# Kernel optimization log

Hardware: AMD Instinct MI355X
Metric: run time of the kernel (lower is better)

Reference implementation:

```python
import jax, jax.numpy as jnp
import numpy as np

NEG_SLOPE = 0.2
EPS = 1e-16


def gat_layer(x, edge_index, edge_attr, W, We, a_src, a_dst, a_edge, bias,
              add_self_loops):
    """PyG GATConv with concat=True.
    x: [N, F_in], edge_index: [2, E] (row 0 = src j, row 1 = dst i),
    edge_attr: [E, De], W: [F_in, H*C], We: [De, H*C],
    a_src/a_dst/a_edge: [H, C], bias: [H*C].
    """
    N = x.shape[0]
    H, C = a_src.shape
    if add_self_loops:
        # fill_value='mean': self-loop edge_attr = mean of incoming edge_attr per node
        dst0 = edge_index[1]
        s = jax.ops.segment_sum(edge_attr, dst0, num_segments=N)
        cnt = jax.ops.segment_sum(jnp.ones((edge_attr.shape[0], 1), edge_attr.dtype),
                                  dst0, num_segments=N)
        loop_attr = s / jnp.maximum(cnt, 1.0)
        loop_idx = jnp.arange(N, dtype=edge_index.dtype)
        edge_index = jnp.concatenate(
            [edge_index, jnp.stack([loop_idx, loop_idx])], axis=1)
        edge_attr = jnp.concatenate([edge_attr, loop_attr], axis=0)

    src, dst = edge_index[0], edge_index[1]
    h = (x @ W).reshape(N, H, C)                       # [N, H, C]
    e = (edge_attr @ We).reshape(-1, H, C)             # [E, H, C]

    alpha_src = jnp.einsum('nhc,hc->nh', h, a_src)     # [N, H]
    alpha_dst = jnp.einsum('nhc,hc->nh', h, a_dst)     # [N, H]
    alpha_edge = jnp.einsum('ehc,hc->eh', e, a_edge)   # [E, H]

    alpha = alpha_src[src] + alpha_dst[dst] + alpha_edge
    alpha = jax.nn.leaky_relu(alpha, NEG_SLOPE)

    # segment softmax over destination node
    amax = jax.ops.segment_max(alpha, dst, num_segments=N)      # [N, H]
    ex = jnp.exp(alpha - amax[dst])
    denom = jax.ops.segment_sum(ex, dst, num_segments=N)        # [N, H]
    attn = ex / (denom[dst] + EPS)                               # [E, H]

    msg = h[src] * attn[:, :, None]                              # [E, H, C]
    out = jax.ops.segment_sum(msg, dst, num_segments=N)          # [N, H, C]
    return out.reshape(N, H * C) + bias


def setup_inputs() -> dict:
    key = jax.random.key(0)
    ks = jax.random.split(key, 16)
    N, E, F_in, C, H, De = 10000, 160000, 128, 64, 8, 1
    d1 = H * C  # 512

    def glorot(k, shape):
        fan = shape[0] + shape[-1]
        s = jnp.sqrt(6.0 / fan)
        return jax.random.uniform(k, shape, jnp.float32, -s, s)

    return {
        'x': jax.random.normal(ks[0], (N, F_in), jnp.float32),
        'edge_index': jax.random.randint(ks[1], (2, E), 0, N, jnp.int32),
        'edge_attr': jax.random.normal(ks[2], (E, De), jnp.float32),
        # layer 1 params
        'W1': glorot(ks[3], (F_in, d1)),
        'We1': glorot(ks[4], (De, d1)),
        'as1': glorot(ks[5], (H, C)),
        'ad1': glorot(ks[6], (H, C)),
        'ae1': glorot(ks[7], (H, C)),
        'b1': jnp.zeros((d1,), jnp.float32),
        # layer 2 params
        'W2': glorot(ks[8], (d1, d1)),
        'We2': glorot(ks[9], (De, d1)),
        'as2': glorot(ks[10], (H, C)),
        'ad2': glorot(ks[11], (H, C)),
        'ae2': glorot(ks[12], (H, C)),
        'b2': jnp.zeros((d1,), jnp.float32),
    }


def reference(x, edge_index, edge_attr,
              W1, We1, as1, ad1, ae1, b1,
              W2, We2, as2, ad2, ae2, b2):
    h = gat_layer(x, edge_index, edge_attr, W1, We1, as1, ad1, ae1, b1,
                  add_self_loops=False)
    h = jax.nn.relu(h)
    h = gat_layer(h, edge_index, edge_attr, W2, We2, as2, ad2, ae2, b2,
                  add_self_loops=True)
    return jnp.mean(h, axis=0)  # [512]
```

## Files before the change

### kernel.cpp

```cpp
#include <hip/hip_runtime.h>
#include <hip/hip_bf16.h>

#define HD __device__ __forceinline__
typedef unsigned short u16;
typedef __attribute__((ext_vector_type(8))) short bf16x8;
typedef __attribute__((ext_vector_type(4))) float f32x4;

HD u16 f2b(float f){
  unsigned u = __float_as_uint(f);
  unsigned r = (u + 0x7fffu + ((u>>16)&1u)) >> 16;
  return (u16)r;
}
HD float b2f(short s){ return __uint_as_float(((unsigned)(u16)s)<<16); }

__global__ void k_count(const int* __restrict__ dst, const float* __restrict__ ea,
                        int* cnt, float* easum, int E){
  int e = blockIdx.x*blockDim.x + threadIdx.x;
  if (e>=E) return;
  int d = dst[e];
  atomicAdd(&cnt[d],1);
  atomicAdd(&easum[d], ea[e]);
}

__global__ __launch_bounds__(1024) void k_scan(const int* __restrict__ cnt, int* offs, int N){
  __shared__ int lds[1024];
  const int chunk = (N + 1023)/1024;
  const int b = threadIdx.x*chunk;
  int s = 0;
  for (int i=0;i<chunk;++i){ int idx=b+i; if (idx<N) s += cnt[idx]; }
  lds[threadIdx.x] = s;
  __syncthreads();
  #pragma unroll
  for (int off=1; off<1024; off<<=1){
    int t = (threadIdx.x>=(unsigned)off)? lds[threadIdx.x-off] : 0;
    __syncthreads();
    lds[threadIdx.x] += t;
    __syncthreads();
  }
  int excl = lds[threadIdx.x] - s;
  for (int i=0;i<chunk;++i){
    int idx=b+i;
    if (idx<N){ offs[idx] = excl; excl += cnt[idx]; }
  }
  if (threadIdx.x==1023) offs[N] = lds[1023];
}

__global__ void k_scatter(const int* __restrict__ src, const int* __restrict__ dst,
                          const float* __restrict__ ea, const int* __restrict__ offs,
                          int* fill, int* srcs, float* eas, int E){
  int e = blockIdx.x*blockDim.x + threadIdx.x;
  if (e>=E) return;
  int d = dst[e];
  int p = offs[d] + atomicAdd(&fill[d],1);
  srcs[p] = src[e];
  eas[p]  = ea[e];
}

__global__ __launch_bounds__(512) void k_prep_small(
    const int* __restrict__ cnt, const float* __restrict__ easum, float* la, int N,
    const float* __restrict__ We1, const float* __restrict__ ae1,
    const float* __restrict__ We2, const float* __restrict__ ae2,
    float* wedot, int nbLoop){
  int bx = blockIdx.x;
  if (bx < nbLoop){
    int n = bx*512 + threadIdx.x;
    if (n<N) la[n] = easum[n] / fmaxf((float)cnt[n], 1.f);
    return;
  }
  int which = bx - nbLoop;
  const float* We = which? We2 : We1;
  const float* ae = which? ae2 : ae1;
  int hh = threadIdx.x>>6, lane = threadIdx.x&63;
  float p = We[hh*64+lane]*ae[hh*64+lane];
  #pragma unroll
  for (int o=32;o;o>>=1) p += __shfl_down(p,o);
  if (lane==0) wedot[which*8+hh] = p;
}

__global__ __launch_bounds__(256) void k_prep_cast(
    const float* __restrict__ x, u16* __restrict__ xb, int total4,
    const float* __restrict__ W1, u16* __restrict__ W1t,
    const float* __restrict__ W2, u16* __restrict__ W2t,
    int nbCast, int nbW1){
  __shared__ float T[64][65];
  int bx = blockIdx.x;
  if (bx < nbCast){
    int i = bx*256 + threadIdx.x;
    if (i<total4){
      float4 v = *(const float4*)(x + (size_t)i*4);
      ushort4 o; o.x=f2b(v.x); o.y=f2b(v.y); o.z=f2b(v.z); o.w=f2b(v.w);
      *(ushort4*)(xb + (size_t)i*4) = o;
    }
    return;
  }
  const float* W; u16* Wt; int K, Nn, t;
  if (bx < nbCast + nbW1){ t = bx - nbCast;        W = W1; Wt = W1t; K = 128; Nn = 512; }
  else                   { t = bx - nbCast - nbW1; W = W2; Wt = W2t; K = 512; Nn = 512; }
  int nt = Nn/64;
  int k0 = (t/nt)*64, n0 = (t%nt)*64;
  #pragma unroll
  for (int i=0;i<16;++i){
    int id = i*256 + threadIdx.x;
    int r = id>>6, c = id&63;
    T[r][c] = W[(size_t)(k0+r)*Nn + n0 + c];
  }
  __syncthreads();
  #pragma unroll
  for (int i=0;i<16;++i){
    int id = i*256 + threadIdx.x;
    int rr = id>>6, cc = id&63;
    Wt[(size_t)(n0+rr)*K + k0 + cc] = f2b(T[cc][rr]);
  }
}

__global__ __launch_bounds__(256) void k_gemm_mfma(
    const u16* __restrict__ A, const u16* __restrict__ Bt,
    u16* __restrict__ Cb,
    const float* __restrict__ a_s, const float* __restrict__ a_d,
    float* __restrict__ asrc, float* __restrict__ adst,
    int M, int N, int K){
  __shared__ char lds[256*80];
  char* As = lds;
  char* Bs = lds + 128*80;
  const int tid = threadIdx.x;
  const int lane = tid & 63, w = tid >> 6;
  const int wr = w >> 1, wc = w & 1;
  const int l15 = lane & 15, l4 = lane >> 4;
  const int m0 = blockIdx.y*128, n0 = blockIdx.x*128;

  f32x4 acc[4][4] = {};
  int aoff[4], boff[4];
  #pragma unroll
  for (int i=0;i<4;++i) aoff[i] = (wr*64 + i*16 + l15)*80 + l4*16;
  #pragma unroll
  for (int j=0;j<4;++j) boff[j] = (wc*64 + j*16 + l15)*80 + l4*16;

  for (int k0=0; k0<K; k0+=32){
    #pragma unroll
    for (int i=0;i<2;++i){
      int cid = tid*2+i;
      int r = cid>>2, c = cid&3;
      int row = m0 + r;
      float4 v = make_float4(0.f,0.f,0.f,0.f);
      if (row < M) v = *(const float4*)(A + (size_t)row*K + k0 + c*8);
      *(float4*)(As + r*80 + c*16) = v;
    }
    #pragma unroll
    for (int i=0;i<2;++i){
      int cid = tid*2+i;
      int r = cid>>2, c = cid&3;
      float4 v = *(const float4*)(Bt + (size_t)(n0+r)*K + k0 + c*8);
      *(float4*)(Bs + r*80 + c*16) = v;
    }
    __syncthreads();
    bf16x8 a[4], b[4];
    #pragma unroll
    for (int i=0;i<4;++i) a[i] = *reinterpret_cast<const bf16x8*>(As + aoff[i]);
    #pragma unroll
    for (int j=0;j<4;++j) b[j] = *reinterpret_cast<const bf16x8*>(Bs + boff[j]);
    #pragma unroll
    for (int i=0;i<4;++i)
      #pragma unroll
      for (int j=0;j<4;++j)
        acc[i][j] = __builtin_amdgcn_mfma_f32_16x16x32_bf16(a[i], b[j], acc[i][j], 0,0,0);
    __syncthreads();
  }

  const int head = (n0>>6) + wc;
  float sv[4][4] = {}, dv[4][4] = {};
  #pragma unroll
  for (int i=0;i<4;++i){
    #pragma unroll
    for (int j=0;j<4;++j){
      int col = n0 + wc*64 + j*16 + l15;
      float asv = a_s[col], adv = a_d[col];
      #pragma unroll
      for (int r=0;r<4;++r){
        int row = m0 + wr*64 + i*16 + l4*4 + r;
        u16 bits = f2b(acc[i][j][r]);
        float valf = b2f((short)bits);
        if (row < M) Cb[(size_t)row*N + col] = bits;
        sv[i][r] = fmaf(valf, asv, sv[i][r]);
        dv[i][r] = fmaf(valf, adv, dv[i][r]);
      }
    }
  }
  #pragma unroll
  for (int i=0;i<4;++i){
    #pragma unroll
    for (int r=0;r<4;++r){
      float s_ = sv[i][r], d_ = dv[i][r];
      #pragma unroll
      for (int mask=1; mask<16; mask<<=1){
        s_ += __shfl_xor(s_, mask);
        d_ += __shfl_xor(d_, mask);
      }
      if (l15==0){
        int row = m0 + wr*64 + i*16 + l4*4 + r;
        if (row < M){ asrc[row*8+head] = s_; adst[row*8+head] = d_; }
      }
    }
  }
}

__global__ __launch_bounds__(256) void k_flashagg(const u16* __restrict__ hb,
    const int* __restrict__ srcs, const float* __restrict__ eas,
    const int* __restrict__ offs,
    const float* __restrict__ asrc, const float* __restrict__ adst,
    const float* __restrict__ wedot, const float* __restrict__ la,
    const float* __restrict__ bias,
    u16* __restrict__ outb,
    int N, int relu_flag, int self_flag){
  int n = blockIdx.x*4 + (threadIdx.x>>6);
  if (n>=N) return;
  int lane = threadIdx.x&63;
  int hh = lane&7, esub = lane>>3;
  int ahh = lane>>3;
  int c0 = lane*8;
  int beg = offs[n], end = offs[n+1];
  float wd = wedot[hh];
  float adn = adst[n*8+hh];

  float aselfa = -1e30f;
  if (self_flag){
    float a = asrc[n*8+hh] + adn + la[n]*wd;
    aselfa = a>0.f ? a : 0.2f*a;
  }
  float aself_c = __shfl(aselfa, ahh);

  float m = self_flag ? aself_c : -1e30f;
  float s = 0.f;
  float acc[8] = {};

  for (int p0=beg; p0<end; p0+=16){
    int pA = p0 + esub, pB = p0 + 8 + esub;
    float aA = -1e30f, aB = -1e30f;
    int sA = 0, sB = 0;
    if (pA < end){
      sA = srcs[pA];
      float eaA = eas[pA];
      float a = asrc[sA*8+hh] + adn + eaA*wd;
      aA = a>0.f ? a : 0.2f*a;
    }
    if (pB < end){
      sB = srcs[pB];
      float eaB = eas[pB];
      float a = asrc[sB*8+hh] + adn + eaB*wd;
      aB = a>0.f ? a : 0.2f*a;
    }
    float av[16]; int se[16];
    #pragma unroll
    for (int e=0;e<8;++e){ av[e]   = __shfl(aA, e*8 + ahh); se[e]   = __shfl(sA, e*8); }
    #pragma unroll
    for (int e=0;e<8;++e){ av[8+e] = __shfl(aB, e*8 + ahh); se[8+e] = __shfl(sB, e*8); }
    float mo = m;
    #pragma unroll
    for (int e=0;e<16;++e) mo = fmaxf(mo, av[e]);
    float f = __expf(m - mo);
    m = mo;
    s *= f;
    #pragma unroll
    for (int j=0;j<8;++j) acc[j] *= f;
    #pragma unroll
    for (int e=0;e<16;++e){
      if (p0 + e < end){
        float ee = __expf(av[e] - m);
        s += ee;
        bf16x8 v = *(const bf16x8*)(hb + (size_t)se[e]*512 + c0);
        #pragma unroll
        for (int j=0;j<8;++j) acc[j] = fmaf(ee, b2f(v[j]), acc[j]);
      }
    }
  }
  if (self_flag){
    float xs = __expf(aself_c - m);
    s += xs;
    bf16x8 v = *(const bf16x8*)(hb + (size_t)n*512 + c0);
    #pragma unroll
    for (int j=0;j<8;++j) acc[j] = fmaf(xs, b2f(v[j]), acc[j]);
  }
  float iv = 1.f/(s + 1e-16f);
  bf16x8 ov;
  #pragma unroll
  for (int j=0;j<8;++j){
    float val = acc[j]*iv + bias[c0+j];
    if (relu_flag) val = fmaxf(val, 0.f);
    ov[j] = (short)f2b(val);
  }
  *(bf16x8*)(outb + (size_t)n*512 + c0) = ov;
}

__global__ __launch_bounds__(512) void k_colmean(const u16* __restrict__ out2b,
                          float* __restrict__ o, int N, float invN){
  int c = threadIdx.x;
  int n0 = blockIdx.x*16;
  int nend = min(n0+16, N);
  float s = 0.f;
  for (int n=n0;n<nend;++n) s += b2f(out2b[(size_t)n*512 + c]);
  atomicAdd(&o[c], s*invN);
}

extern "C" void kernel_launch(void* const* d_in, const int* in_sizes, int n_in,
                              void* d_out, int out_size, void* d_ws, size_t ws_size,
                              hipStream_t stream){
  const float* x   = (const float*)d_in[0];
  const int* eidx  = (const int*)d_in[1];
  const float* ea  = (const float*)d_in[2];
  const float* W1  = (const float*)d_in[3];
  const float* We1 = (const float*)d_in[4];
  const float* as1 = (const float*)d_in[5];
  const float* ad1 = (const float*)d_in[6];
  const float* ae1 = (const float*)d_in[7];
  const float* b1  = (const float*)d_in[8];
  const float* W2  = (const float*)d_in[9];
  const float* We2 = (const float*)d_in[10];
  const float* as2 = (const float*)d_in[11];
  const float* ad2 = (const float*)d_in[12];
  const float* ae2 = (const float*)d_in[13];
  const float* b2  = (const float*)d_in[14];
  float* outp = (float*)d_out;

  const int FIN = 128, D1 = 512;
  const int N = in_sizes[0]/FIN;
  const int E = in_sizes[1]/2;
  const int* srcA = eidx;
  const int* dstA = eidx + E;

  char* ws = (char*)d_ws;
  size_t o = 0;
  auto alloc = [&](size_t bytes)->void*{
    void* p = ws + o; o = (o + bytes + 255) & ~(size_t)255; return p;
  };
  u16*   hb1   = (u16*)  alloc((size_t)N*D1*2);
  u16*   hb2   = (u16*)  alloc((size_t)N*D1*2);
  u16*   out1rb= (u16*)  alloc((size_t)N*D1*2);
  u16*   out2b = (u16*)  alloc((size_t)N*D1*2);
  u16*   xb    = (u16*)  alloc((size_t)N*FIN*2);
  u16*   W1t   = (u16*)  alloc((size_t)D1*FIN*2);
  u16*   W2t   = (u16*)  alloc((size_t)D1*D1*2);
  int*   srcs  = (int*)  alloc((size_t)E*4);
  float* eas   = (float*)alloc((size_t)E*4);
  int*   offs  = (int*)  alloc((size_t)(N+1)*4);
  size_t zbeg = o;
  int*   cnt   = (int*)  alloc((size_t)N*4);
  int*   fill  = (int*)  alloc((size_t)N*4);
  float* easum = (float*)alloc((size_t)N*4);
  size_t zend = o;
  float* asrc  = (float*)alloc((size_t)N*8*4);
  float* adst  = (float*)alloc((size_t)N*8*4);
  float* la    = (float*)alloc((size_t)N*4);
  float* wedot = (float*)alloc(64);
  (void)ws_size; (void)n_in;

  hipMemsetAsync(ws + zbeg, 0, zend - zbeg, stream);
  hipMemsetAsync(d_out, 0, (size_t)out_size*sizeof(float), stream);

  dim3 b256(256);
  int ge = (E+255)/256;
  int gn4 = (N+3)/4;

  k_count   <<<ge, b256, 0, stream>>>(dstA, ea, cnt, easum, E);
  k_scan    <<<1, 1024, 0, stream>>>(cnt, offs, N);
  k_scatter <<<ge, b256, 0, stream>>>(srcA, dstA, ea, offs, fill, srcs, eas, E);
  {
    int nbLoop = (N+511)/512;
    k_prep_small<<<nbLoop+2, 512, 0, stream>>>(cnt, easum, la, N,
                                               We1, ae1, We2, ae2, wedot, nbLoop);
    int total4 = N*FIN/4;
    int nbCast = (total4+255)/256;
    int nbW1 = (FIN/64)*(D1/64);
    int nbW2 = (D1/64)*(D1/64);
    k_prep_cast<<<nbCast+nbW1+nbW2, b256, 0, stream>>>(x, xb, total4,
                                                       W1, W1t, W2, W2t, nbCast, nbW1);
  }

  k_gemm_mfma<<<dim3(D1/128, (N+127)/128), b256, 0, stream>>>(
      xb, W1t, hb1, as1, ad1, asrc, adst, N, D1, FIN);
  k_flashagg<<<gn4, b256, 0, stream>>>(hb1, srcs, eas, offs, asrc, adst, wedot, la,
                                       b1, out1rb, N, 1, 0);

  k_gemm_mfma<<<dim3(D1/128, (N+127)/128), b256, 0, stream>>>(
      out1rb, W2t, hb2, as2, ad2, asrc, adst, N, D1, D1);
  k_flashagg<<<gn4, b256, 0, stream>>>(hb2, srcs, eas, offs, asrc, adst, wedot+8, la,
                                       b2, out2b, N, 0, 1);

  k_colmean<<<(N+15)/16, 512, 0, stream>>>(out2b, outp, N, 1.0f/(float)N);
}
```

Measured before the change: 179.8 us.

## Merge prep kernels and fuse x bf16 cast into first GEMM load

Merges edge counting, weight transpose/cast and wedot computation into one launch, and runs the scan, loop-attr mean and first GEMM together in a second launch. The first GEMM now reads fp32 x directly and rounds to bf16 while staging tiles, which removes the separate cast pass and the xb buffer. The scan shrinks to a single 256-thread block inside the heterogeneous launch, so it does less parallel work per element and can become the longest block. The aim is to cut launch count and serial dependencies in the preprocessing phase.

```diff
diff --git a/kernel.cpp b/kernel.cpp
--- a/kernel.cpp
+++ b/kernel.cpp
@@ -13,120 +13,19 @@
 }
 HD float b2f(short s){ return __uint_as_float(((unsigned)(u16)s)<<16); }
 
-__global__ void k_count(const int* __restrict__ dst, const float* __restrict__ ea,
-                        int* cnt, float* easum, int E){
-  int e = blockIdx.x*blockDim.x + threadIdx.x;
-  if (e>=E) return;
-  int d = dst[e];
-  atomicAdd(&cnt[d],1);
-  atomicAdd(&easum[d], ea[e]);
-}
-
-__global__ __launch_bounds__(1024) void k_scan(const int* __restrict__ cnt, int* offs, int N){
-  __shared__ int lds[1024];
-  const int chunk = (N + 1023)/1024;
-  const int b = threadIdx.x*chunk;
-  int s = 0;
-  for (int i=0;i<chunk;++i){ int idx=b+i; if (idx<N) s += cnt[idx]; }
-  lds[threadIdx.x] = s;
-  __syncthreads();
-  #pragma unroll
-  for (int off=1; off<1024; off<<=1){
-    int t = (threadIdx.x>=(unsigned)off)? lds[threadIdx.x-off] : 0;
-    __syncthreads();
-    lds[threadIdx.x] += t;
-    __syncthreads();
-  }
-  int excl = lds[threadIdx.x] - s;
-  for (int i=0;i<chunk;++i){
-    int idx=b+i;
-    if (idx<N){ offs[idx] = excl; excl += cnt[idx]; }
-  }
-  if (threadIdx.x==1023) offs[N] = lds[1023];
-}
-
-__global__ void k_scatter(const int* __restrict__ src, const int* __restrict__ dst,
-                          const float* __restrict__ ea, const int* __restrict__ offs,
-                          int* fill, int* srcs, float* eas, int E){
-  int e = blockIdx.x*blockDim.x + threadIdx.x;
-  if (e>=E) return;
-  int d = dst[e];
-  int p = offs[d] + atomicAdd(&fill[d],1);
-  srcs[p] = src[e];
-  eas[p]  = ea[e];
-}
-
-__global__ __launch_bounds__(512) void k_prep_small(
-    const int* __restrict__ cnt, const float* __restrict__ easum, float* la, int N,
-    const float* __restrict__ We1, const float* __restrict__ ae1,
-    const float* __restrict__ We2, const float* __restrict__ ae2,
-    float* wedot, int nbLoop){
-  int bx = blockIdx.x;
-  if (bx < nbLoop){
-    int n = bx*512 + threadIdx.x;
-    if (n<N) la[n] = easum[n] / fmaxf((float)cnt[n], 1.f);
-    return;
-  }
-  int which = bx - nbLoop;
-  const float* We = which? We2 : We1;
-  const float* ae = which? ae2 : ae1;
-  int hh = threadIdx.x>>6, lane = threadIdx.x&63;
-  float p = We[hh*64+lane]*ae[hh*64+lane];
-  #pragma unroll
-  for (int o=32;o;o>>=1) p += __shfl_down(p,o);
-  if (lane==0) wedot[which*8+hh] = p;
-}
-
-__global__ __launch_bounds__(256) void k_prep_cast(
-    const float* __restrict__ x, u16* __restrict__ xb, int total4,
-    const float* __restrict__ W1, u16* __restrict__ W1t,
-    const float* __restrict__ W2, u16* __restrict__ W2t,
-    int nbCast, int nbW1){
-  __shared__ float T[64][65];
-  int bx = blockIdx.x;
-  if (bx < nbCast){
-    int i = bx*256 + threadIdx.x;
-    if (i<total4){
-      float4 v = *(const float4*)(x + (size_t)i*4);
-      ushort4 o; o.x=f2b(v.x); o.y=f2b(v.y); o.z=f2b(v.z); o.w=f2b(v.w);
-      *(ushort4*)(xb + (size_t)i*4) = o;
-    }
-    return;
-  }
-  const float* W; u16* Wt; int K, Nn, t;
-  if (bx < nbCast + nbW1){ t = bx - nbCast;        W = W1; Wt = W1t; K = 128; Nn = 512; }
-  else                   { t = bx - nbCast - nbW1; W = W2; Wt = W2t; K = 512; Nn = 512; }
-  int nt = Nn/64;
-  int k0 = (t/nt)*64, n0 = (t%nt)*64;
-  #pragma unroll
-  for (int i=0;i<16;++i){
-    int id = i*256 + threadIdx.x;
-    int r = id>>6, c = id&63;
-    T[r][c] = W[(size_t)(k0+r)*Nn + n0 + c];
-  }
-  __syncthreads();
-  #pragma unroll
-  for (int i=0;i<16;++i){
-    int id = i*256 + threadIdx.x;
-    int rr = id>>6, cc = id&63;
-    Wt[(size_t)(n0+rr)*K + k0 + cc] = f2b(T[cc][rr]);
-  }
-}
-
-__global__ __launch_bounds__(256) void k_gemm_mfma(
-    const u16* __restrict__ A, const u16* __restrict__ Bt,
-    u16* __restrict__ Cb,
-    const float* __restrict__ a_s, const float* __restrict__ a_d,
-    float* __restrict__ asrc, float* __restrict__ adst,
-    int M, int N, int K){
-  __shared__ char lds[256*80];
+template<int AF32>
+HD void gemm_body(const void* Ap, const u16* __restrict__ Bt,
+                  u16* __restrict__ Cb,
+                  const float* __restrict__ a_s, const float* __restrict__ a_d,
+                  float* __restrict__ asrc, float* __restrict__ adst,
+                  int M, int N, int K, int bidx, int bidy, char* lds){
   char* As = lds;
   char* Bs = lds + 128*80;
   const int tid = threadIdx.x;
   const int lane = tid & 63, w = tid >> 6;
   const int wr = w >> 1, wc = w & 1;
   const int l15 = lane & 15, l4 = lane >> 4;
-  const int m0 = blockIdx.y*128, n0 = blockIdx.x*128;
+  const int m0 = bidy*128, n0 = bidx*128;
 
   f32x4 acc[4][4] = {};
   int aoff[4], boff[4];
@@ -141,9 +40,24 @@
       int cid = tid*2+i;
       int r = cid>>2, c = cid&3;
       int row = m0 + r;
-      float4 v = make_float4(0.f,0.f,0.f,0.f);
-      if (row < M) v = *(const float4*)(A + (size_t)row*K + k0 + c*8);
-      *(float4*)(As + r*80 + c*16) = v;
+      if (AF32){
+        const float* A = (const float*)Ap;
+        float4 v0 = make_float4(0.f,0.f,0.f,0.f), v1 = v0;
+        if (row < M){
+          v0 = *(const float4*)(A + (size_t)row*K + k0 + c*8);
+          v1 = *(const float4*)(A + (size_t)row*K + k0 + c*8 + 4);
+        }
+        ushort4 o0, o1;
+        o0.x=f2b(v0.x); o0.y=f2b(v0.y); o0.z=f2b(v0.z); o0.w=f2b(v0.w);
+        o1.x=f2b(v1.x); o1.y=f2b(v1.y); o1.z=f2b(v1.z); o1.w=f2b(v1.w);
+        *(ushort4*)(As + r*80 + c*16)     = o0;
+        *(ushort4*)(As + r*80 + c*16 + 8) = o1;
+      } else {
+        const u16* A = (const u16*)Ap;
+        float4 v = make_float4(0.f,0.f,0.f,0.f);
+        if (row < M) v = *(const float4*)(A + (size_t)row*K + k0 + c*8);
+        *(float4*)(As + r*80 + c*16) = v;
+      }
     }
     #pragma unroll
     for (int i=0;i<2;++i){
@@ -201,6 +115,125 @@
       }
     }
   }
+}
+
+__global__ __launch_bounds__(256) void k_prepA(
+    const int* __restrict__ dst, const float* __restrict__ ea,
+    int* cnt, float* easum, int E, int nbCount,
+    const float* __restrict__ W1, u16* __restrict__ W1t,
+    const float* __restrict__ W2, u16* __restrict__ W2t,
+    const float* __restrict__ We1, const float* __restrict__ ae1,
+    const float* __restrict__ We2, const float* __restrict__ ae2,
+    float* wedot){
+  __shared__ float T[64][65];
+  int bx = blockIdx.x;
+  int tid = threadIdx.x;
+  if (bx < nbCount){
+    int e = bx*256 + tid;
+    if (e<E){
+      int d = dst[e];
+      atomicAdd(&cnt[d],1);
+      atomicAdd(&easum[d], ea[e]);
+    }
+    return;
+  }
+  bx -= nbCount;
+  if (bx < 16 + 64){
+    const float* W; u16* Wt; int K, t;
+    if (bx < 16){ t = bx;      W = W1; Wt = W1t; K = 128; }
+    else        { t = bx - 16; W = W2; Wt = W2t; K = 512; }
+    const int Nn = 512, nt = 8;
+    int k0 = (t/nt)*64, n0 = (t%nt)*64;
+    #pragma unroll
+    for (int i=0;i<16;++i){
+      int id = i*256 + tid;
+      int r = id>>6, c = id&63;
+      T[r][c] = W[(size_t)(k0+r)*Nn + n0 + c];
+    }
+    __syncthreads();
+    #pragma unroll
+    for (int i=0;i<16;++i){
+      int id = i*256 + tid;
+      int rr = id>>6, cc = id&63;
+      Wt[(size_t)(n0+rr)*K + k0 + cc] = f2b(T[cc][rr]);
+    }
+    return;
+  }
+  int idx = bx - 80;
+  int which = idx>>1, hg = idx&1;
+  const float* We = which? We2 : We1;
+  const float* ae = which? ae2 : ae1;
+  int wv = tid>>6, lane = tid&63;
+  int head = hg*4 + wv;
+  float p = We[head*64+lane]*ae[head*64+lane];
+  #pragma unroll
+  for (int o=32;o;o>>=1) p += __shfl_down(p,o);
+  if (lane==0) wedot[which*8+head] = p;
+}
+
+__global__ __launch_bounds__(256) void k_prepB(
+    const int* __restrict__ cnt, int* offs, int N, int nbLa,
+    const float* __restrict__ easum, float* la,
+    const float* __restrict__ x, const u16* __restrict__ W1t,
+    u16* __restrict__ hb1,
+    const float* __restrict__ a_s, const float* __restrict__ a_d,
+    float* __restrict__ asrc, float* __restrict__ adst,
+    int M, int Nd, int K){
+  __shared__ char glds[256*80];
+  __shared__ int slds[256];
+  int bx = blockIdx.x;
+  int tid = threadIdx.x;
+  if (bx == 0){
+    const int chunk = (N + 255)/256;
+    const int b = tid*chunk;
+    int s = 0;
+    for (int i=0;i<chunk;++i){ int idx=b+i; if (idx<N) s += cnt[idx]; }
+    slds[tid] = s;
+    __syncthreads();
+    #pragma unroll
+    for (int off=1; off<256; off<<=1){
+      int t = (tid>=off)? slds[tid-off] : 0;
+      __syncthreads();
+      slds[tid] += t;
+      __syncthreads();
+    }
+    int excl = slds[tid] - s;
+    for (int i=0;i<chunk;++i){
+      int idx=b+i;
+      if (idx<N){ offs[idx] = excl; excl += cnt[idx]; }
+    }
+    if (tid==255) offs[N] = slds[255];
+    return;
+  }
+  if (bx < 1 + nbLa){
+    int n = (bx-1)*256 + tid;
+    if (n<N) la[n] = easum[n] / fmaxf((float)cnt[n], 1.f);
+    return;
+  }
+  int t = bx - 1 - nbLa;
+  gemm_body<1>(x, W1t, hb1, a_s, a_d, asrc, adst, M, Nd, K, t%4, t/4, glds);
+}
+
+__global__ void k_scatter(const int* __restrict__ src, const int* __restrict__ dst,
+                          const float* __restrict__ ea, const int* __restrict__ offs,
+                          int* fill, int* srcs, float* eas, int E){
+  int e = blockIdx.x*blockDim.x + threadIdx.x;
+  if (e>=E) return;
+  int d = dst[e];
+  int p = offs[d] + atomicAdd(&fill[d],1);
+  srcs[p] = src[e];
+  eas[p]  = ea[e];
+}
+
+__global__ __launch_bounds__(256) void k_gemm_mfma(
+    const u16* __restrict__ A, const u16* __restrict__ Bt,
+    u16* __restrict__ Cb,
+    const float* __restrict__ a_s, const float* __restrict__ a_d,
+    float* __restrict__ asrc, float* __restrict__ adst,
+    int M, int N, int K){
+  __shared__ char lds[256*80];
+  gemm_body<0>(A, Bt, Cb, a_s, a_d, asrc, adst, M, N, K,
+               blockIdx.x, blockIdx.y, lds);
 }
 
 __global__ __launch_bounds__(256) void k_flashagg(const u16* __restrict__ hb,
@@ -335,7 +368,6 @@
   u16*   hb2   = (u16*)  alloc((size_t)N*D1*2);
   u16*   out1rb= (u16*)  alloc((size_t)N*D1*2);
   u16*   out2b = (u16*)  alloc((size_t)N*D1*2);
-  u16*   xb    = (u16*)  alloc((size_t)N*FIN*2);
   u16*   W1t   = (u16*)  alloc((size_t)D1*FIN*2);
   u16*   W2t   = (u16*)  alloc((size_t)D1*D1*2);
   int*   srcs  = (int*)  alloc((size_t)E*4);
@@ -359,28 +391,25 @@
   int ge = (E+255)/256;
   int gn4 = (N+3)/4;
 
-  k_count   <<<ge, b256, 0, stream>>>(dstA, ea, cnt, easum, E);
-  k_scan    <<<1, 1024, 0, stream>>>(cnt, offs, N);
-  k_scatter <<<ge, b256, 0, stream>>>(srcA, dstA, ea, offs, fill, srcs, eas, E);
-  {
-    int nbLoop = (N+511)/512;
-    k_prep_small<<<nbLoop+2, 512, 0, stream>>>(cnt, easum, la, N,
-                                               We1, ae1, We2, ae2, wedot, nbLoop);
-    int total4 = N*FIN/4;
-    int nbCast = (total4+255)/256;
-    int nbW1 = (FIN/64)*(D1/64);
-    int nbW2 = (D1/64)*(D1/64);
-    k_prep_cast<<<nbCast+nbW1+nbW2, b256, 0, stream>>>(x, xb, total4,
-                                                       W1, W1t, W2, W2t, nbCast, nbW1);
-  }
-
-  k_gemm_mfma<<<dim3(D1/128, (N+127)/128), b256, 0, stream>>>(
-      xb, W1t, hb1, as1, ad1, asrc, adst, N, D1, FIN);
+  int nbCount = ge;
+  k_prepA<<<nbCount + 16 + 64 + 4, b256, 0, stream>>>(
+      dstA, ea, cnt, easum, E, nbCount,
+      W1, W1t, W2, W2t, We1, ae1, We2, ae2, wedot);
+
+  int nbLa = (N+255)/256;
+  int nbG1 = (D1/128)*((N+127)/128);
+  k_prepB<<<1 + nbLa + nbG1, b256, 0, stream>>>(
+      cnt, offs, N, nbLa, easum, la,
+      x, W1t, hb1, as1, ad1, asrc, adst, N, D1, FIN);
+
+  k_scatter<<<ge, b256, 0, stream>>>(srcA, dstA, ea, offs, fill, srcs, eas, E);
+
   k_flashagg<<<gn4, b256, 0, stream>>>(hb1, srcs, eas, offs, asrc, adst, wedot, la,
                                        b1, out1rb, N, 1, 0);
 
   k_gemm_mfma<<<dim3(D1/128, (N+127)/128), b256, 0, stream>>>(
       out1rb, W2t, hb2, as2, ad2, asrc, adst, N, D1, D1);
+
   k_flashagg<<<gn4, b256, 0, stream>>>(hb2, srcs, eas, offs, asrc, adst, wedot+8, la,
                                        b2, out2b, N, 0, 1);
 
```

Result: faster. 175.2 us (-2.6%).
